# Optimization experiments

Hardware: AMD Instinct MI355X
Metric: run time of the kernel (lower is better)

The kernel has to match this reference:

```python
import jax, jax.numpy as jnp
import numpy as np

DIM = 768
HEADS = 12
HEAD_DIM = DIM // HEADS
HIDDEN = int(DIM * 4.0)
EPS = 1e-5
SCALE = HEAD_DIM ** -0.5


def _layernorm(x, g, b):
    m = jnp.mean(x, axis=-1, keepdims=True)
    v = jnp.mean(jnp.square(x - m), axis=-1, keepdims=True)
    return (x - m) * jax.lax.rsqrt(v + EPS) * g + b


def setup_inputs() -> dict:
    key = jax.random.key(0)
    ks = jax.random.split(key, 12)
    B, N = 2, 2048
    s = 0.02
    return {
        "x": jax.random.normal(ks[0], (B, N, DIM), dtype=jnp.float32),
        "mask": jax.random.randint(ks[1], (B, N), 0, 2, dtype=jnp.int32),
        "ln1_g": jnp.ones((DIM,), jnp.float32),
        "ln1_b": jnp.zeros((DIM,), jnp.float32),
        "qkv_w": jax.random.normal(ks[2], (3 * DIM, DIM), jnp.float32) * s,
        "proj_w": jax.random.normal(ks[3], (DIM, DIM), jnp.float32) * s,
        "proj_b": jnp.zeros((DIM,), jnp.float32),
        "ln2_g": jnp.ones((DIM,), jnp.float32),
        "ln2_b": jnp.zeros((DIM,), jnp.float32),
        "fc1_w": jax.random.normal(ks[4], (HIDDEN, DIM), jnp.float32) * s,
        "fc1_b": jnp.zeros((HIDDEN,), jnp.float32),
        "fc2_w": jax.random.normal(ks[5], (DIM, HIDDEN), jnp.float32) * s,
        "fc2_b": jnp.zeros((DIM,), jnp.float32),
    }


def reference(x, mask, ln1_g, ln1_b, qkv_w, proj_w, proj_b, ln2_g, ln2_b,
              fc1_w, fc1_b, fc2_w, fc2_b):
    B, N, C = x.shape
    # --- attention on norm1(x) ---
    h = _layernorm(x, ln1_g, ln1_b)
    qkv = (h @ qkv_w.T).reshape(B, N, 3, HEADS, HEAD_DIM)
    q, k, v = qkv[:, :, 0], qkv[:, :, 1], qkv[:, :, 2]  # [B,N,H,D]
    scores = jnp.einsum('bnhd,bmhd->bhnm', q, k) * SCALE  # [B,H,N,N]
    neg_inf = jnp.finfo(scores.dtype).min
    scores = jnp.where(mask[:, None, None, :] == 1, neg_inf, scores)
    attn = jax.nn.softmax(scores, axis=-1)
    y = jnp.einsum('bhnm,bmhd->bnhd', attn, v).reshape(B, N, C)
    y = y @ proj_w.T + proj_b
    x = x + y
    # --- MLP on norm2(x) ---
    h2 = _layernorm(x, ln2_g, ln2_b)
    h2 = jax.nn.gelu(h2 @ fc1_w.T + fc1_b, approximate=False)
    x = x + (h2 @ fc2_w.T + fc2_b)
    return x
```

## Files before the change

### kernel.cpp

```cpp
#include <hip/hip_runtime.h>
#include <math.h>
#include <float.h>

#define DIM 768
#define HEADS 12
#define HD 64
#define HIDDEN 3072
#define SEQ 2048
#define BATCH 2
#define NTOK (BATCH * SEQ)
#define QKVC (3 * DIM)
#define LN_EPS 1e-5f
#define SC2 0.1803368801111f

typedef unsigned short u16;
typedef __attribute__((ext_vector_type(8))) __bf16 bf16x8;
typedef __attribute__((ext_vector_type(8))) unsigned short u16x8;
typedef __attribute__((ext_vector_type(4))) float f32x4;

__device__ __forceinline__ u16 f2bf(float f) {
    unsigned int u = __builtin_bit_cast(unsigned int, f);
    u += 0x7fffu + ((u >> 16) & 1u);
    return (u16)(u >> 16);
}

__device__ __forceinline__ f32x4 mfma16(u16x8 a, u16x8 b, f32x4 c) {
    return __builtin_amdgcn_mfma_f32_16x16x32_bf16(
        __builtin_bit_cast(bf16x8, a), __builtin_bit_cast(bf16x8, b), c, 0, 0, 0);
}

__device__ __forceinline__ void gl2lds16(const void* g, void* l) {
    __builtin_amdgcn_global_load_lds(
        (const __attribute__((address_space(1))) void*)g,
        (__attribute__((address_space(3))) void*)l, 16, 0, 0);
}

__device__ __forceinline__ float gelu_f(float v) {
    return 0.5f * v * (1.0f + erff(v * 0.70710678118654752f));
}

__global__ __launch_bounds__(256) void cvt_all(const float* __restrict__ qkvw,
                                               const float* __restrict__ projw,
                                               const float* __restrict__ fc1w,
                                               const float* __restrict__ fc2w,
                                               u16* __restrict__ o_qkv,
                                               u16* __restrict__ o_proj,
                                               u16* __restrict__ o_fc1,
                                               u16* __restrict__ o_fc2,
                                               const int* __restrict__ mask,
                                               int* __restrict__ pos,
                                               int* __restrict__ cnt) {
    if (blockIdx.x >= 6912) {
        int b = blockIdx.x - 6912, t = threadIdx.x;
        const int* m = mask + b * SEQ;
        int v[8], s = 0;
#pragma unroll
        for (int j = 0; j < 8; ++j) { v[j] = (m[t * 8 + j] == 1) ? 0 : 1; s += v[j]; }
        __shared__ int red[256];
        red[t] = s;
        __syncthreads();
        for (int off = 1; off < 256; off <<= 1) {
            int x = (t >= off) ? red[t - off] : 0;
            __syncthreads();
            red[t] += x;
            __syncthreads();
        }
        int base = red[t] - s;
#pragma unroll
        for (int j = 0; j < 8; ++j) {
            pos[b * SEQ + t * 8 + j] = v[j] ? base : -1;
            base += v[j];
        }
        if (t == 255) cnt[b] = red[255];
        return;
    }
    long i = (long)(blockIdx.x * 256 + threadIdx.x) * 4;
    const float* s; u16* d; long off;
    if (i < 1769472)      { s = qkvw;  d = o_qkv;  off = i; }
    else if (i < 2359296) { s = projw; d = o_proj; off = i - 1769472; }
    else if (i < 4718592) { s = fc1w;  d = o_fc1;  off = i - 2359296; }
    else                  { s = fc2w;  d = o_fc2;  off = i - 4718592; }
    float4 v = *(const float4*)(s + off);
    ushort4 o;
    o.x = f2bf(v.x); o.y = f2bf(v.y); o.z = f2bf(v.z); o.w = f2bf(v.w);
    *(ushort4*)(d + off) = o;
}

__global__ __launch_bounds__(256) void ln_kernel(const float* __restrict__ x,
                                                 const float* __restrict__ g,
                                                 const float* __restrict__ bta,
                                                 u16* __restrict__ out) {
    int row = blockIdx.x;
    int t = threadIdx.x;
    const float* xr = x + (size_t)row * DIM;
    float v0 = xr[t], v1 = xr[t + 256], v2 = xr[t + 512];
    __shared__ float red[256];
    red[t] = v0 + v1 + v2;
    __syncthreads();
    for (int off = 128; off > 0; off >>= 1) {
        if (t < off) red[t] += red[t + off];
        __syncthreads();
    }
    float mean = red[0] * (1.0f / DIM);
    __syncthreads();
    float d0 = v0 - mean, d1 = v1 - mean, d2 = v2 - mean;
    red[t] = d0 * d0 + d1 * d1 + d2 * d2;
    __syncthreads();
    for (int off = 128; off > 0; off >>= 1) {
        if (t < off) red[t] += red[t + off];
        __syncthreads();
    }
    float rstd = rsqrtf(red[0] * (1.0f / DIM) + LN_EPS);
    u16* orow = out + (size_t)row * DIM;
    orow[t]       = f2bf(d0 * rstd * g[t]       + bta[t]);
    orow[t + 256] = f2bf(d1 * rstd * g[t + 256] + bta[t + 256]);
    orow[t + 512] = f2bf(d2 * rstd * g[t + 512] + bta[t + 512]);
}

__global__ __launch_bounds__(256) void repack_kv(const u16* __restrict__ qkv,
                                                 const int* __restrict__ pos,
                                                 u16* __restrict__ kh,
                                                 u16* __restrict__ vth) {
    int s = blockIdx.x;
    int bh = blockIdx.y;
    int b = bh / HEADS, h = bh % HEADS;
    int t = threadIdx.x;
    __shared__ u16 Vl[64 * 72];
    __shared__ int lpos[64];
    const u16* base = qkv + ((size_t)(b * SEQ + s * 64)) * QKVC + h * HD;
    if (t < 64) lpos[t] = pos[b * SEQ + s * 64 + t];
    {
        int vkey = (t & 31) * 2, vd0 = (t >> 5) * 8;
        const u16* g0 = base + 2 * DIM + (size_t)vkey * QKVC + vd0;
        u16x8 a = *(const u16x8*)g0;
        u16x8 c = *(const u16x8*)(g0 + QKVC);
#pragma unroll
        for (int j = 0; j < 8; ++j) {
            unsigned int pk = (unsigned int)a[j] | ((unsigned int)c[j] << 16);
            *(unsigned int*)(Vl + (vd0 + j) * 72 + vkey) = pk;
        }
    }
    __syncthreads();
    {
        int r = t >> 2, d0 = (t & 3) * 16;
        int p = lpos[r];
        if (p >= 0) {
            const u16* g = base + DIM + (size_t)r * QKVC + d0;
            u16* o = kh + (size_t)bh * (SEQ * HD) + (size_t)p * HD + d0;
            *(uint4*)o = *(const uint4*)g;
            *(uint4*)(o + 8) = *(const uint4*)(g + 8);
        }
    }
    {
        int d = t >> 2, m0 = (t & 3) * 16;
        u16* orow = vth + (size_t)bh * (HD * SEQ) + (size_t)d * SEQ;
#pragma unroll
        for (int j = 0; j < 16; ++j) {
            int p = lpos[m0 + j];
            if (p >= 0) orow[p] = Vl[d * 72 + m0 + j];
        }
    }
}

template <int BM, int BN, int EPI>
__global__ __launch_bounds__(256) void mgemm(const u16* __restrict__ A,
                                             const u16* __restrict__ Bw,
                                             void* __restrict__ Cout,
                                             void* __restrict__ Cout2,
                                             int N, int klen,
                                             const float* __restrict__ bias,
                                             const float* __restrict__ resid) {
    constexpr int WM = BM / 2, WN = BN / 2, NI = WM / 16, NJ = WN / 16;
    constexpr int ACALLS = (BM * 128) / 4096;
    constexpr int BCALLS = (BN * 128) / 4096;
    __shared__ u16 As[BM * 64];
    __shared__ u16 Bs[BN * 64];
    int t = threadIdx.x;
    int w = t >> 6, lane = t & 63;
    int quad = lane >> 4, m16 = lane & 15;
    int bx = blockIdx.x, by = blockIdx.y;
    if (EPI == 4) {
        int gx = gridDim.x;
        int flat = by * gx + bx;
        bx = (flat >> 3) % gx;
        by = (flat & 7) + 8 * ((flat >> 3) / gx);
    }
    int K = klen * gridDim.z;
    int kbeg = blockIdx.z * klen;
    int row0 = by * BM, col0 = bx * BN;
    int lrow = lane >> 3;
    int lk = (lane & 7) ^ lrow;

    f32x4 acc[NI][NJ] = {};

    for (int k0 = kbeg; k0 < kbeg + klen; k0 += 64) {
        __syncthreads();
#pragma unroll
        for (int c = 0; c < ACALLS; ++c) {
            int r = (w * ACALLS + c) * 8 + lrow;
            const u16* g = A + (size_t)(row0 + r) * K + k0 + lk * 8;
            gl2lds16(g, As + (w * ACALLS + c) * 512);
        }
#pragma unroll
        for (int c = 0; c < BCALLS; ++c) {
            int r = (w * BCALLS + c) * 8 + lrow;
            const u16* g = Bw + (size_t)(col0 + r) * K + k0 + lk * 8;
            gl2lds16(g, Bs + (w * BCALLS + c) * 512);
        }
        __syncthreads();
#pragma unroll
        for (int ks = 0; ks < 2; ++ks) {
            u16x8 af[NI], bfj[NJ];
#pragma unroll
            for (int i = 0; i < NI; ++i) {
                int rowL = (w >> 1) * WM + 16 * i + m16;
                af[i] = *(const u16x8*)(As + rowL * 64 +
                                        (((ks * 4 + quad) ^ (rowL & 7)) * 8));
            }
#pragma unroll
            for (int j = 0; j < NJ; ++j) {
                int rowL = (w & 1) * WN + 16 * j + m16;
                bfj[j] = *(const u16x8*)(Bs + rowL * 64 +
                                         (((ks * 4 + quad) ^ (rowL & 7)) * 8));
            }
#pragma unroll
            for (int i = 0; i < NI; ++i)
#pragma unroll
                for (int j = 0; j < NJ; ++j)
                    acc[i][j] = mfma16(af[i], bfj[j], acc[i][j]);
        }
    }

    int wr0 = row0 + (w >> 1) * WM, wc0 = col0 + (w & 1) * WN;
#pragma unroll
    for (int i = 0; i < NI; ++i)
#pragma unroll
        for (int j = 0; j < NJ; ++j) {
            int ccol = wc0 + 16 * j + m16;
#pragma unroll
            for (int r = 0; r < 4; ++r) {
                int crow = wr0 + 16 * i + quad * 4 + r;
                float v = acc[i][j][r];
                if (EPI == 0) {
                    ((u16*)Cout)[(size_t)crow * N + ccol] = f2bf(v);
                } else if (EPI == 1) {
                    v += bias[ccol] + resid[(size_t)crow * N + ccol];
                    ((float*)Cout)[(size_t)crow * N + ccol] = v;
                } else if (EPI == 2) {
                    v = gelu_f(v + bias[ccol]);
                    ((u16*)Cout)[(size_t)crow * N + ccol] = f2bf(v);
                } else {
                    if (blockIdx.z == 0) {
                        ((float*)Cout)[(size_t)crow * N + ccol] = v;
                    } else {
                        v += bias[ccol] + resid[(size_t)crow * N + ccol];
                        ((float*)Cout2)[(size_t)crow * N + ccol] = v;
                    }
                }
            }
        }
}

__global__ __launch_bounds__(256) void merge_kernel(float* __restrict__ out,
                                                    const float* __restrict__ part) {
    int i = (blockIdx.x * 256 + threadIdx.x) * 4;
    float4 o = *(const float4*)(out + i);
    float4 p = *(const float4*)(part + i);
    o.x += p.x; o.y += p.y; o.z += p.z; o.w += p.w;
    *(float4*)(out + i) = o;
}

__global__ __launch_bounds__(256, 3) void attn_mfma(const u16* __restrict__ qkv,
                                                    const u16* __restrict__ kh,
                                                    const u16* __restrict__ vth,
                                                    const int* __restrict__ cnt,
                                                    u16* __restrict__ y) {
    int gx = gridDim.x;
    int flat = blockIdx.y * gx + blockIdx.x;
    int qt = (flat >> 3) % gx;
    int bh = (flat & 7) + 8 * ((flat >> 3) / gx);
    int b = bh / HEADS, h = bh % HEADS;
    int t = threadIdx.x, w = t >> 6, lane = t & 63;
    int quad = lane >> 4, m16 = lane & 15;
    __shared__ u16 Ks[128 * 64];
    __shared__ u16 Vt[64 * 128];
    __shared__ u16 Pw[4][16 * 136];
    const u16* kbase = kh + (size_t)bh * (SEQ * HD);
    const u16* vbase = vth + (size_t)bh * (SEQ * HD);

    int qrow = b * SEQ + qt * 64 + w * 16 + m16;
    const u16* qp = qkv + (size_t)qrow * QKVC + h * HD + quad * 8;
    u16x8 qf0 = *(const u16x8*)qp;
    u16x8 qf1 = *(const u16x8*)(qp + 32);

    int rloc = lane >> 3, kslot = lane & 7;
    int kchunk = kslot ^ rloc;
    int dloc = lane >> 4, vslot = lane & 15;

    float lsum[4] = {0.f, 0.f, 0.f, 0.f};
    f32x4 O[4] = {};

    int slo = quad ^ (m16 & 7);

    int cntb = cnt[b];
    int ntile = (cntb + 127) >> 7;

    for (int kt = 0; kt < ntile; ++kt) {
        int k0 = kt << 7;
        __syncthreads();
#pragma unroll
        for (int c = 0; c < 4; ++c) {
            int rb = (w * 4 + c) * 8;
            const u16* g = kbase + (size_t)(k0 + rb + rloc) * HD + kchunk * 8;
            gl2lds16(g, Ks + (w * 4 + c) * 512);
        }
#pragma unroll
        for (int c = 0; c < 4; ++c) {
            int d = (w * 4 + c) * 4 + dloc;
            int chunk = vslot ^ (d & 15);
            const u16* g = vbase + (size_t)d * SEQ + k0 + chunk * 8;
            gl2lds16(g, Vt + (w * 4 + c) * 512);
        }
        float kb[8];
#pragma unroll
        for (int nb = 0; nb < 8; ++nb)
            kb[nb] = (k0 + m16 + 16 * nb < cntb) ? 0.0f : -1e30f;
        __syncthreads();

#pragma unroll
        for (int nb = 0; nb < 8; ++nb) {
            const u16* krow = Ks + (m16 + 16 * nb) * 64;
            f32x4 s = {0.f, 0.f, 0.f, 0.f};
            s = mfma16(qf0, *(const u16x8*)(krow + slo * 8), s);
            s = mfma16(qf1, *(const u16x8*)(krow + (slo ^ 4) * 8), s);
#pragma unroll
            for (int r = 0; r < 4; ++r) {
                float p = __builtin_amdgcn_exp2f(s[r] * SC2 + kb[nb]);
                lsum[r] += p;
                Pw[w][(quad * 4 + r) * 136 + m16 + 16 * nb] = f2bf(p);
            }
        }
        u16x8 pf[4];
#pragma unroll
        for (int ks = 0; ks < 4; ++ks)
            pf[ks] = *(const u16x8*)(Pw[w] + m16 * 136 + ks * 32 + quad * 8);
#pragma unroll
        for (int nbd = 0; nbd < 4; ++nbd) {
            const u16* vrow = Vt + (nbd * 16 + m16) * 128;
#pragma unroll
            for (int ks = 0; ks < 4; ++ks) {
                int sl = (quad + 4 * ks) ^ m16;
                O[nbd] = mfma16(pf[ks], *(const u16x8*)(vrow + sl * 8), O[nbd]);
            }
        }
    }
#pragma unroll
    for (int off = 1; off < 16; off <<= 1)
#pragma unroll
        for (int r = 0; r < 4; ++r)
            lsum[r] += __shfl_xor(lsum[r], off);
#pragma unroll
    for (int r = 0; r < 4; ++r) {
        float inv = 1.0f / lsum[r];
        int tok = b * SEQ + qt * 64 + w * 16 + quad * 4 + r;
        u16* yr = y + (size_t)tok * DIM + h * HD + m16;
#pragma unroll
        for (int nbd = 0; nbd < 4; ++nbd) yr[16 * nbd] = f2bf(O[nbd][r] * inv);
    }
}

extern "C" void kernel_launch(void* const* d_in, const int* in_sizes, int n_in,
                              void* d_out, int out_size, void* d_ws, size_t ws_size,
                              hipStream_t stream) {
    const float* x      = (const float*)d_in[0];
    const int*   mask   = (const int*)d_in[1];
    const float* ln1_g  = (const float*)d_in[2];
    const float* ln1_b  = (const float*)d_in[3];
    const float* qkv_w  = (const float*)d_in[4];
    const float* proj_w = (const float*)d_in[5];
    const float* proj_b = (const float*)d_in[6];
    const float* ln2_g  = (const float*)d_in[7];
    const float* ln2_b  = (const float*)d_in[8];
    const float* fc1_w  = (const float*)d_in[9];
    const float* fc1_b  = (const float*)d_in[10];
    const float* fc2_w  = (const float*)d_in[11];
    const float* fc2_b  = (const float*)d_in[12];
    float* out = (float*)d_out;

    char* W = (char*)d_ws;
    u16*   wqkv  = (u16*)(W + 0);
    u16*   wproj = (u16*)(W + 3538944);
    u16*   wfc1  = (u16*)(W + 4718592);
    u16*   wfc2  = (u16*)(W + 9437184);
    u16*   hbuf  = (u16*)(W + 14155776);
    float* x1    = (float*)(W + 20447232);
    int*   posb  = (int*)(W + 20463616);
    int*   cntb  = (int*)(W + 20480000);
    u16*   qkvb  = (u16*)(W + 33030144);
    u16*   ybuf  = (u16*)(W + 51904512);
    u16*   a1    = (u16*)(W + 33030144);
    u16*   khb   = (u16*)(W + 58212352);
    u16*   vthb  = (u16*)(W + 64503808);
    float* pp    = (float*)(W + 58212352);

    cvt_all<<<6914, 256, 0, stream>>>(qkv_w, proj_w, fc1_w, fc2_w,
                                      wqkv, wproj, wfc1, wfc2,
                                      mask, posb, cntb);

    ln_kernel<<<NTOK, 256, 0, stream>>>(x, ln1_g, ln1_b, hbuf);
    mgemm<128, 128, 0><<<dim3(QKVC / 128, NTOK / 128), 256, 0, stream>>>(
        hbuf, wqkv, qkvb, nullptr, QKVC, DIM, nullptr, nullptr);
    repack_kv<<<dim3(SEQ / 64, BATCH * HEADS), 256, 0, stream>>>(qkvb, posb, khb, vthb);
    attn_mfma<<<dim3(SEQ / 64, BATCH * HEADS), 256, 0, stream>>>(
        qkvb, khb, vthb, cntb, ybuf);
    mgemm<128, 64, 1><<<dim3(DIM / 64, NTOK / 128), 256, 0, stream>>>(
        ybuf, wproj, x1, nullptr, DIM, DIM, proj_b, x);
    ln_kernel<<<NTOK, 256, 0, stream>>>(x1, ln2_g, ln2_b, hbuf);
    mgemm<128, 128, 2><<<dim3(HIDDEN / 128, NTOK / 128), 256, 0, stream>>>(
        hbuf, wfc1, a1, nullptr, HIDDEN, DIM, fc1_b, nullptr);
    mgemm<128, 64, 4><<<dim3(DIM / 64, NTOK / 128, 2), 256, 0, stream>>>(
        a1, wfc2, pp, out, DIM, HIDDEN / 2, fc2_b, x1);
    merge_kernel<<<NTOK * DIM / 1024, 256, 0, stream>>>(out, pp);
}
```

Baseline: 264.7 us.

## Fold LN1 into conversion kernel, warp-per-row layernorm, and tunable GEMM K-tile

LN1 now runs inside the weight-conversion/mask-prefix launch as extra blocks, one wavefront per row using float4 loads and shuffle reductions, which removes a separate launch. LN2 uses the same warp-per-row routine in place of the shared-memory tree reduction. The GEMM template gains a BK parameter with a matching swizzle. The proj GEMM moves to 64x64 tiles with BK=128, giving more blocks, and fc2 uses BK=128 to halve the number of barrier iterations. Larger BK increases LDS use per block and may reduce occupancy.

Result: no change. 263.4 us (-0.5%).

```diff
diff --git a/kernel.cpp b/kernel.cpp
--- a/kernel.cpp
+++ b/kernel.cpp
@@ -39,6 +39,41 @@
     return 0.5f * v * (1.0f + erff(v * 0.70710678118654752f));
 }
 
+__device__ __forceinline__ void ln_row(const float* __restrict__ xr,
+                                       const float* __restrict__ g,
+                                       const float* __restrict__ bta,
+                                       u16* __restrict__ orow, int lane) {
+    float4 v0 = *(const float4*)(xr + lane * 4);
+    float4 v1 = *(const float4*)(xr + 256 + lane * 4);
+    float4 v2 = *(const float4*)(xr + 512 + lane * 4);
+    float s = v0.x + v0.y + v0.z + v0.w + v1.x + v1.y + v1.z + v1.w +
+              v2.x + v2.y + v2.z + v2.w;
+#pragma unroll
+    for (int off = 1; off < 64; off <<= 1) s += __shfl_xor(s, off);
+    float mean = s * (1.0f / DIM);
+    float d[12] = {v0.x - mean, v0.y - mean, v0.z - mean, v0.w - mean,
+                   v1.x - mean, v1.y - mean, v1.z - mean, v1.w - mean,
+                   v2.x - mean, v2.y - mean, v2.z - mean, v2.w - mean};
+    float q = 0.f;
+#pragma unroll
+    for (int i = 0; i < 12; ++i) q += d[i] * d[i];
+#pragma unroll
+    for (int off = 1; off < 64; off <<= 1) q += __shfl_xor(q, off);
+    float rstd = rsqrtf(q * (1.0f / DIM) + LN_EPS);
+#pragma unroll
+    for (int p = 0; p < 3; ++p) {
+        int col = p * 256 + lane * 4;
+        float4 gg = *(const float4*)(g + col);
+        float4 bb = *(const float4*)(bta + col);
+        ushort4 o;
+        o.x = f2bf(d[p * 4 + 0] * rstd * gg.x + bb.x);
+        o.y = f2bf(d[p * 4 + 1] * rstd * gg.y + bb.y);
+        o.z = f2bf(d[p * 4 + 2] * rstd * gg.z + bb.z);
+        o.w = f2bf(d[p * 4 + 3] * rstd * gg.w + bb.w);
+        *(ushort4*)(orow + col) = o;
+    }
+}
+
 __global__ __launch_bounds__(256) void cvt_all(const float* __restrict__ qkvw,
                                                const float* __restrict__ projw,
                                                const float* __restrict__ fc1w,
@@ -49,7 +84,17 @@
                                                u16* __restrict__ o_fc2,
                                                const int* __restrict__ mask,
                                                int* __restrict__ pos,
-                                               int* __restrict__ cnt) {
+                                               int* __restrict__ cnt,
+                                               const float* __restrict__ x,
+                                               const float* __restrict__ ln1_g,
+                                               const float* __restrict__ ln1_b,
+                                               u16* __restrict__ hbuf) {
+    if (blockIdx.x >= 6914) {
+        int w = threadIdx.x >> 6, lane = threadIdx.x & 63;
+        int row = (blockIdx.x - 6914) * 4 + w;
+        ln_row(x + (size_t)row * DIM, ln1_g, ln1_b, hbuf + (size_t)row * DIM, lane);
+        return;
+    }
     if (blockIdx.x >= 6912) {
         int b = blockIdx.x - 6912, t = threadIdx.x;
         const int* m = mask + b * SEQ;
@@ -60,9 +105,9 @@
         red[t] = s;
         __syncthreads();
         for (int off = 1; off < 256; off <<= 1) {
-            int x = (t >= off) ? red[t - off] : 0;
+            int xv = (t >= off) ? red[t - off] : 0;
             __syncthreads();
-            red[t] += x;
+            red[t] += xv;
             __syncthreads();
         }
         int base = red[t] - s;
@@ -86,35 +131,13 @@
     *(ushort4*)(d + off) = o;
 }
 
-__global__ __launch_bounds__(256) void ln_kernel(const float* __restrict__ x,
-                                                 const float* __restrict__ g,
-                                                 const float* __restrict__ bta,
-                                                 u16* __restrict__ out) {
-    int row = blockIdx.x;
-    int t = threadIdx.x;
-    const float* xr = x + (size_t)row * DIM;
-    float v0 = xr[t], v1 = xr[t + 256], v2 = xr[t + 512];
-    __shared__ float red[256];
-    red[t] = v0 + v1 + v2;
-    __syncthreads();
-    for (int off = 128; off > 0; off >>= 1) {
-        if (t < off) red[t] += red[t + off];
-        __syncthreads();
-    }
-    float mean = red[0] * (1.0f / DIM);
-    __syncthreads();
-    float d0 = v0 - mean, d1 = v1 - mean, d2 = v2 - mean;
-    red[t] = d0 * d0 + d1 * d1 + d2 * d2;
-    __syncthreads();
-    for (int off = 128; off > 0; off >>= 1) {
-        if (t < off) red[t] += red[t + off];
-        __syncthreads();
-    }
-    float rstd = rsqrtf(red[0] * (1.0f / DIM) + LN_EPS);
-    u16* orow = out + (size_t)row * DIM;
-    orow[t]       = f2bf(d0 * rstd * g[t]       + bta[t]);
-    orow[t + 256] = f2bf(d1 * rstd * g[t + 256] + bta[t + 256]);
-    orow[t + 512] = f2bf(d2 * rstd * g[t + 512] + bta[t + 512]);
+__global__ __launch_bounds__(256) void ln2_kernel(const float* __restrict__ x,
+                                                  const float* __restrict__ g,
+                                                  const float* __restrict__ bta,
+                                                  u16* __restrict__ out) {
+    int w = threadIdx.x >> 6, lane = threadIdx.x & 63;
+    int row = blockIdx.x * 4 + w;
+    ln_row(x + (size_t)row * DIM, g, bta, out + (size_t)row * DIM, lane);
 }
 
 __global__ __launch_bounds__(256) void repack_kv(const u16* __restrict__ qkv,
@@ -162,7 +185,7 @@
     }
 }
 
-template <int BM, int BN, int EPI>
+template <int BM, int BN, int BK, int EPI>
 __global__ __launch_bounds__(256) void mgemm(const u16* __restrict__ A,
                                              const u16* __restrict__ Bw,
                                              void* __restrict__ Cout,
@@ -171,10 +194,12 @@
                                              const float* __restrict__ bias,
                                              const float* __restrict__ resid) {
     constexpr int WM = BM / 2, WN = BN / 2, NI = WM / 16, NJ = WN / 16;
-    constexpr int ACALLS = (BM * 128) / 4096;
-    constexpr int BCALLS = (BN * 128) / 4096;
-    __shared__ u16 As[BM * 64];
-    __shared__ u16 Bs[BN * 64];
+    constexpr int CH = BK / 8;
+    constexpr int RPC = 512 / BK;
+    constexpr int ACALLS = (BM * BK) / 2048;
+    constexpr int BCALLS = (BN * BK) / 2048;
+    __shared__ u16 As[BM * BK];
+    __shared__ u16 Bs[BN * BK];
     int t = threadIdx.x;
     int w = t >> 6, lane = t & 63;
     int quad = lane >> 4, m16 = lane & 15;
@@ -188,40 +213,44 @@
     int K = klen * gridDim.z;
     int kbeg = blockIdx.z * klen;
     int row0 = by * BM, col0 = bx * BN;
-    int lrow = lane >> 3;
-    int lk = (lane & 7) ^ lrow;
+    int rloc = lane / CH;
+    int cslot = lane % CH;
 
     f32x4 acc[NI][NJ] = {};
 
-    for (int k0 = kbeg; k0 < kbeg + klen; k0 += 64) {
+    for (int k0 = kbeg; k0 < kbeg + klen; k0 += BK) {
         __syncthreads();
 #pragma unroll
         for (int c = 0; c < ACALLS; ++c) {
-            int r = (w * ACALLS + c) * 8 + lrow;
-            const u16* g = A + (size_t)(row0 + r) * K + k0 + lk * 8;
+            int callrow = (w * ACALLS + c) * RPC;
+            int r = callrow + rloc;
+            int chunk = cslot ^ (r & (CH - 1));
+            const u16* g = A + (size_t)(row0 + r) * K + k0 + chunk * 8;
             gl2lds16(g, As + (w * ACALLS + c) * 512);
         }
 #pragma unroll
         for (int c = 0; c < BCALLS; ++c) {
-            int r = (w * BCALLS + c) * 8 + lrow;
-            const u16* g = Bw + (size_t)(col0 + r) * K + k0 + lk * 8;
+            int callrow = (w * BCALLS + c) * RPC;
+            int r = callrow + rloc;
+            int chunk = cslot ^ (r & (CH - 1));
+            const u16* g = Bw + (size_t)(col0 + r) * K + k0 + chunk * 8;
             gl2lds16(g, Bs + (w * BCALLS + c) * 512);
         }
         __syncthreads();
 #pragma unroll
-        for (int ks = 0; ks < 2; ++ks) {
+        for (int ks = 0; ks < BK / 32; ++ks) {
             u16x8 af[NI], bfj[NJ];
 #pragma unroll
             for (int i = 0; i < NI; ++i) {
                 int rowL = (w >> 1) * WM + 16 * i + m16;
-                af[i] = *(const u16x8*)(As + rowL * 64 +
-                                        (((ks * 4 + quad) ^ (rowL & 7)) * 8));
+                af[i] = *(const u16x8*)(As + rowL * BK +
+                                        (((ks * 4 + quad) ^ (rowL & (CH - 1))) * 8));
             }
 #pragma unroll
             for (int j = 0; j < NJ; ++j) {
                 int rowL = (w & 1) * WN + 16 * j + m16;
-                bfj[j] = *(const u16x8*)(Bs + rowL * 64 +
-                                         (((ks * 4 + quad) ^ (rowL & 7)) * 8));
+                bfj[j] = *(const u16x8*)(Bs + rowL * BK +
+                                         (((ks * 4 + quad) ^ (rowL & (CH - 1))) * 8));
             }
 #pragma unroll
             for (int i = 0; i < NI; ++i)
@@ -403,22 +432,22 @@
     u16*   vthb  = (u16*)(W + 64503808);
     float* pp    = (float*)(W + 58212352);
 
-    cvt_all<<<6914, 256, 0, stream>>>(qkv_w, proj_w, fc1_w, fc2_w,
+    cvt_all<<<7938, 256, 0, stream>>>(qkv_w, proj_w, fc1_w, fc2_w,
                                       wqkv, wproj, wfc1, wfc2,
-                                      mask, posb, cntb);
-
-    ln_kernel<<<NTOK, 256, 0, stream>>>(x, ln1_g, ln1_b, hbuf);
-    mgemm<128, 128, 0><<<dim3(QKVC / 128, NTOK / 128), 256, 0, stream>>>(
+                                      mask, posb, cntb,
+                                      x, ln1_g, ln1_b, hbuf);
+
+    mgemm<128, 128, 64, 0><<<dim3(QKVC / 128, NTOK / 128), 256, 0, stream>>>(
         hbuf, wqkv, qkvb, nullptr, QKVC, DIM, nullptr, nullptr);
     repack_kv<<<dim3(SEQ / 64, BATCH * HEADS), 256, 0, stream>>>(qkvb, posb, khb, vthb);
     attn_mfma<<<dim3(SEQ / 64, BATCH * HEADS), 256, 0, stream>>>(
         qkvb, khb, vthb, cntb, ybuf);
-    mgemm<128, 64, 1><<<dim3(DIM / 64, NTOK / 128), 256, 0, stream>>>(
+    mgemm<64, 64, 128, 1><<<dim3(DIM / 64, NTOK / 64), 256, 0, stream>>>(
         ybuf, wproj, x1, nullptr, DIM, DIM, proj_b, x);
-    ln_kernel<<<NTOK, 256, 0, stream>>>(x1, ln2_g, ln2_b, hbuf);
-    mgemm<128, 128, 2><<<dim3(HIDDEN / 128, NTOK / 128), 256, 0, stream>>>(
+    ln2_kernel<<<NTOK / 4, 256, 0, stream>>>(x1, ln2_g, ln2_b, hbuf);
+    mgemm<128, 128, 64, 2><<<dim3(HIDDEN / 128, NTOK / 128), 256, 0, stream>>>(
         hbuf, wfc1, a1, nullptr, HIDDEN, DIM, fc1_b, nullptr);
-    mgemm<128, 64, 4><<<dim3(DIM / 64, NTOK / 128, 2), 256, 0, stream>>>(
+    mgemm<128, 64, 128, 4><<<dim3(DIM / 64, NTOK / 128, 2), 256, 0, stream>>>(
         a1, wfc2, pp, out, DIM, HIDDEN / 2, fc2_b, x1);
     merge_kernel<<<NTOK * DIM / 1024, 256, 0, stream>>>(out, pp);
 }
```
